# Kernel optimization log

Hardware: AMD Instinct MI355X
Metric: run time of the kernel (lower is better)

The kernel has to match this reference:

```python
import jax, jax.numpy as jnp
import numpy as np

NS, BS, U, NR, NT, D = 256, 7, 8, 4, 8, 2
ITERS, HID = 3, 200
P, NOISE = 100.0, 1e-7
CIN = 2 * NT * D  # block input width: flattened Z1 and Z2


def setup_inputs() -> dict:
    key = jax.random.key(0)
    ks = jax.random.split(key, 21)
    rn = lambda k, s: jax.random.normal(k, s, dtype=jnp.float32)
    inp = {
        'H_re': rn(ks[0], (NS, BS, BS, U, NR, NT)),
        'H_im': rn(ks[1], (NS, BS, BS, U, NR, NT)),
        'V_re': rn(ks[2], (NS, BS, U, NT, D)),
        'V_im': rn(ks[3], (NS, BS, U, NT, D)),
        'w': jnp.ones((U,), jnp.float32),
        'W1_re': rn(ks[4], (ITERS, HID, CIN)) * 0.05,
        'W1_im': rn(ks[5], (ITERS, HID, CIN)) * 0.05,
        'b1_re': rn(ks[6], (ITERS, HID)) * 0.05,
        'b1_im': rn(ks[7], (ITERS, HID)) * 0.05,
        'W2_re': rn(ks[8], (ITERS, HID, HID)) * 0.05,
        'W2_im': rn(ks[9], (ITERS, HID, HID)) * 0.05,
        'b2_re': rn(ks[10], (ITERS, HID)) * 0.05,
        'b2_im': rn(ks[11], (ITERS, HID)) * 0.05,
        'W3_re': rn(ks[12], (ITERS, HID, HID)) * 0.05,
        'W3_im': rn(ks[13], (ITERS, HID, HID)) * 0.05,
        'b3_re': rn(ks[14], (ITERS, HID)) * 0.05,
        'b3_im': rn(ks[15], (ITERS, HID)) * 0.05,
        'W4_re': rn(ks[16], (ITERS, 1, HID)) * 0.05,
        'W4_im': rn(ks[17], (ITERS, 1, HID)) * 0.05,
        'b4_re': rn(ks[18], (ITERS, 1)) * 0.05,
        'b4_im': rn(ks[19], (ITERS, 1)) * 0.05,
    }
    return inp


def _crelu(x):
    # ComplexReLU: relu on real part, imaginary part passes through
    return jax.nn.relu(x.real) + 1j * x.imag


def _clin(x, W, b):
    # torch Linear with complex weights: x @ W.T + b
    return jnp.einsum('...i,oi->...o', x, W) + b


def _iteration(H, V, w, p):
    n = H.shape[0]
    Z = V
    # HV[n,k,l,i,j] = H[n,k,l,i] @ V[n,k,j]  -> [n,BS,BS,U,U,NR,D]
    HV = jnp.einsum('nklirt,nkjtd->nklijrd', H, V)
    ab = jnp.arange(BS)
    au = jnp.arange(U)
    HV2 = HV[:, ab, ab][:, :, au, au]  # HV[:,k,k,i,i] -> [n,BS,U,NR,D]
    # T[n,k,l,i,j] = HV @ HV^H -> [n,BS,BS,U,U,NR,NR]
    T = jnp.einsum('nklijrd,nklijsd->nklijrs', HV, HV.conj())
    I_r = jnp.eye(NR, dtype=HV.dtype)
    # U[n,l,u] = noise*I + sum_{k,j} T[n,k,l,u,j]
    Usum = NOISE * I_r + T.sum(axis=(1, 4))  # [n,BS,U,NR,NR]
    Y = jnp.linalg.solve(Usum, HV2)
    Td = T[:, ab, ab][:, :, au, au]  # T[:,l,l,u,u]
    F = Usum - Td
    Gamma = jnp.einsum('nlurd,nlure->nlude', HV2.conj(), jnp.linalg.solve(F, HV2))
    IG = jnp.eye(D, dtype=HV.dtype) + Gamma  # [n,BS,U,D,D]
    # A[n,l,m,u] = H[n,l,m,u].mH @ Y[n,m,u] -> [n,BS,BS,U,NT,D]
    A = jnp.einsum('nlmurt,nmurd->nlmutd', H.conj(), Y)
    # L[n,l,u] = sum_m A @ IG[m,u] @ A^H -> [n,BS,U,NT,NT]
    L = jnp.einsum('nlmutd,nmude,nlmuse->nluts', A, IG, A.conj())
    All = A[:, ab, ab]  # A[:,l,l] -> [n,BS,U,NT,D]
    Lam = jnp.einsum('nlutd,nlude->nlute', All, IG)
    wv = w.astype(HV.dtype)[None, None, :, None, None]
    Lam = Lam * wv
    L = L * wv
    Z2 = Lam - jnp.einsum('nluts,nlusd->nlutd', L, Z)
    inp = jnp.concatenate([Z.reshape(n, BS, U, NT * D), Z2.reshape(n, BS, U, NT * D)], -1)
    W1, b1, W2, b2, W3, b3, W4, b4 = p
    h = _crelu(_clin(inp, W1, b1))
    h = _crelu(_clin(h, W2, b2))
    h = _crelu(_clin(h, W3, b3))
    step = _clin(h, W4, b4).real  # [n,BS,U,1]
    Vn = Z + step[..., None] * Z2
    fro = (jnp.abs(Vn) ** 2).sum((-2, -1)).sum(2)  # [n,BS]
    scale = jnp.where(fro > P, jnp.sqrt(P / fro), 1.0)
    return Vn * scale[:, :, None, None, None].astype(Vn.dtype)


def reference(H_re, H_im, V_re, V_im, w, W1_re, W1_im, b1_re, b1_im, W2_re, W2_im, b2_re, b2_im, W3_re, W3_im, b3_re, b3_im, W4_re, W4_im, b4_re, b4_im):
    H = (H_re + 1j * H_im).astype(jnp.complex64)
    V = (V_re + 1j * V_im).astype(jnp.complex64)
    # init_input power normalization per (sample, BS)
    fro0 = (jnp.abs(V) ** 2).sum((-2, -1)).sum(2)
    V = V * jnp.sqrt(P / fro0)[:, :, None, None, None].astype(V.dtype)
    c64 = jnp.complex64
    Ws = [(W1_re + 1j * W1_im).astype(c64), (b1_re + 1j * b1_im).astype(c64),
          (W2_re + 1j * W2_im).astype(c64), (b2_re + 1j * b2_im).astype(c64),
          (W3_re + 1j * W3_im).astype(c64), (b3_re + 1j * b3_im).astype(c64),
          (W4_re + 1j * W4_im).astype(c64), (b4_re + 1j * b4_im).astype(c64)]
    for it in range(ITERS):
        p = tuple(a[it] for a in Ws)
        V = _iteration(H, V, w, p)
    return jnp.stack([V.real, V.imag], axis=-1)
```

## Files before the change

### kernel.cpp

```cpp
#include <hip/hip_runtime.h>
#include <math.h>

#define NS 256
#define BS 7
#define UU 8
#define NR 4
#define NT 8
#define DD 2
#define HID 200
#define CIN 32
#define PP 100.0f
#define NOISEF 1e-7f

typedef _Float16 f16x8 __attribute__((ext_vector_type(8)));
typedef float f32x4 __attribute__((ext_vector_type(4)));

#define AST 424
#define AST0 104
#define NTILES 28
#define B1_KC 3
#define B23_KC 13
#define B1_HALVES (B1_KC*NTILES*64*8)
#define B23_HALVES (B23_KC*NTILES*64*8)
#define BITER_HALVES (B1_HALVES + 2*B23_HALVES)

__device__ void chol_solve(const float2 (*A)[NR], const float2 (*B)[DD], float2 (*X)[DD]) {
  float2 L[NR][NR];
  for (int j = 0; j < NR; ++j) {
    float d = A[j][j].x;
    for (int k = 0; k < j; ++k) d -= L[j][k].x * L[j][k].x + L[j][k].y * L[j][k].y;
    float ld = sqrtf(fmaxf(d, 1e-30f));
    L[j][j] = make_float2(ld, 0.f);
    float inv = 1.f / ld;
    for (int i = j + 1; i < NR; ++i) {
      float sr = A[i][j].x, si = A[i][j].y;
      for (int k = 0; k < j; ++k) {
        float2 a = L[i][k], b = L[j][k];
        sr -= a.x * b.x + a.y * b.y;
        si -= a.y * b.x - a.x * b.y;
      }
      L[i][j] = make_float2(sr * inv, si * inv);
    }
  }
  for (int c = 0; c < DD; ++c) {
    float2 z[NR];
    for (int i = 0; i < NR; ++i) {
      float sr = B[i][c].x, si = B[i][c].y;
      for (int k = 0; k < i; ++k) {
        float2 a = L[i][k], zz = z[k];
        sr -= a.x * zz.x - a.y * zz.y;
        si -= a.x * zz.y + a.y * zz.x;
      }
      float inv = 1.f / L[i][i].x;
      z[i] = make_float2(sr * inv, si * inv);
    }
    for (int i = NR - 1; i >= 0; --i) {
      float sr = z[i].x, si = z[i].y;
      for (int k = i + 1; k < NR; ++k) {
        float2 a = L[k][i], xx = X[k][c];
        sr -= a.x * xx.x + a.y * xx.y;
        si -= a.x * xx.y - a.y * xx.x;
      }
      float inv = 1.f / L[i][i].x;
      X[i][c] = make_float2(sr * inv, si * inv);
    }
  }
}

__global__ void k_norm0(const float* __restrict__ Vre, const float* __restrict__ Vim,
                        float2* __restrict__ Vcur) {
  int nl = blockIdx.x;
  int tid = threadIdx.x;
  size_t base = (size_t)nl * 128;
  float re = Vre[base + tid], im = Vim[base + tid];
  float p = re * re + im * im;
  p += __shfl_down(p, 32); p += __shfl_down(p, 16); p += __shfl_down(p, 8);
  p += __shfl_down(p, 4);  p += __shfl_down(p, 2);  p += __shfl_down(p, 1);
  __shared__ float sred[2];
  if ((tid & 63) == 0) sred[tid >> 6] = p;
  __syncthreads();
  float fro = sred[0] + sred[1];
  float sc = sqrtf(PP / fro);
  Vcur[base + tid] = make_float2(re * sc, im * sc);
}

__global__ __launch_bounds__(512) void k_hv(const float* __restrict__ Hre,
    const float* __restrict__ Him, const float2* __restrict__ Vcur,
    float2* __restrict__ Gsb, float2* __restrict__ Tdb, float2* __restrict__ HV2b) {
  int nl = blockIdx.x; int l = nl % BS; int n = nl / BS;
  int tid = threadIdx.x;
  int wave = tid >> 6;
  int lane = tid & 63;
  int k = lane >> 3, j = lane & 7;

  __shared__ float2 Hs[1820];
  __shared__ float2 Vs[952];

  for (int idx = tid; idx < 1792; idx += 512) {
    int kk = idx >> 8, irt = idx & 255;
    size_t off = ((size_t)(n * BS + kk) * BS + l) * 256 + irt;
    Hs[kk * 260 + irt] = make_float2(Hre[off], Him[off]);
  }
  const float2* Vn = Vcur + (size_t)n * 896;
  for (int idx = tid; idx < 896; idx += 512) {
    int kj = idx >> 4, td = idx & 15;
    Vs[kj * 17 + td] = Vn[idx];
  }
  __syncthreads();

  float2 Gu[10];
  #pragma unroll
  for (int q = 0; q < 10; ++q) Gu[q] = make_float2(0.f, 0.f);
  float2 hv[4][2];
  #pragma unroll
  for (int r = 0; r < 4; ++r)
    #pragma unroll
    for (int d = 0; d < 2; ++d) hv[r][d] = make_float2(0.f, 0.f);

  if (k < 7) {
    float2 v[8][2];
    const float2* vp = &Vs[(k * 8 + j) * 17];
    #pragma unroll
    for (int t = 0; t < 8; ++t) { v[t][0] = vp[2 * t]; v[t][1] = vp[2 * t + 1]; }
    #pragma unroll
    for (int r = 0; r < 4; ++r) {
      const float2* hp = &Hs[k * 260 + wave * 32 + r * 8];
      #pragma unroll
      for (int t = 0; t < 8; ++t) {
        float2 h = hp[t];
        #pragma unroll
        for (int d = 0; d < 2; ++d) {
          hv[r][d].x += h.x * v[t][d].x - h.y * v[t][d].y;
          hv[r][d].y += h.x * v[t][d].y + h.y * v[t][d].x;
        }
      }
    }
    int ui = 0;
    #pragma unroll
    for (int r = 0; r < 4; ++r)
      #pragma unroll
      for (int s = r; s < 4; ++s) {
        float gr = 0.f, gi = 0.f;
        #pragma unroll
        for (int d = 0; d < 2; ++d) {
          float2 a = hv[r][d], c = hv[s][d];
          gr += a.x * c.x + a.y * c.y;
          gi += a.y * c.x - a.x * c.y;
        }
        Gu[ui] = make_float2(gr, gi);
        ++ui;
      }
  }
  if (k == l && j == wave) {
    float2* tdp = Tdb + (size_t)(nl * 8 + wave) * 10;
    #pragma unroll
    for (int q = 0; q < 10; ++q) tdp[q] = Gu[q];
    float2* h2p = HV2b + (size_t)(nl * 8 + wave) * 8;
    #pragma unroll
    for (int x = 0; x < 8; ++x) h2p[x] = hv[x >> 1][x & 1];
  }
  #pragma unroll
  for (int m = 1; m < 64; m <<= 1) {
    #pragma unroll
    for (int q = 0; q < 10; ++q) {
      Gu[q].x += __shfl_xor(Gu[q].x, m);
      Gu[q].y += __shfl_xor(Gu[q].y, m);
    }
  }
  if (lane == 0) {
    float2* gp = Gsb + (size_t)(nl * 8 + wave) * 10;
    #pragma unroll
    for (int q = 0; q < 10; ++q) gp[q] = Gu[q];
  }
}

__global__ __launch_bounds__(256) void k_solve(const float2* __restrict__ Gsb,
    const float2* __restrict__ Tdb, const float2* __restrict__ HV2b,
    float2* __restrict__ Yb, float2* __restrict__ IGb) {
  int gid = blockIdx.x * 256 + threadIdx.x;
  int which = (gid >= 14336) ? 1 : 0;
  int b = gid - which * 14336;

  float2 G[10];
  const float2* gp = Gsb + (size_t)b * 10;
  #pragma unroll
  for (int q = 0; q < 10; ++q) G[q] = gp[q];
  if (which) {
    const float2* tp = Tdb + (size_t)b * 10;
    #pragma unroll
    for (int q = 0; q < 10; ++q) { float2 t = tp[q]; G[q].x -= t.x; G[q].y -= t.y; }
  }
  float2 M[NR][NR];
  {
    int ui = 0;
    #pragma unroll
    for (int r = 0; r < 4; ++r)
      #pragma unroll
      for (int s = r; s < 4; ++s) {
        M[r][s] = G[ui];
        M[s][r] = make_float2(G[ui].x, -G[ui].y);
        ++ui;
      }
    #pragma unroll
    for (int r = 0; r < 4; ++r) { M[r][r].x += NOISEF; M[r][r].y = 0.f; }
  }
  float2 Bv[NR][DD], X[NR][DD];
  const float2* hp = HV2b + (size_t)b * 8;
  #pragma unroll
  for (int x = 0; x < 8; ++x) Bv[x >> 1][x & 1] = hp[x];
  chol_solve(M, Bv, X);
  if (!which) {
    #pragma unroll
    for (int x = 0; x < 8; ++x) Yb[(size_t)b * 8 + x] = X[x >> 1][x & 1];
  } else {
    #pragma unroll
    for (int d = 0; d < DD; ++d)
      #pragma unroll
      for (int e = 0; e < DD; ++e) {
        float gr = (d == e) ? 1.f : 0.f, gi = 0.f;
        #pragma unroll
        for (int r = 0; r < NR; ++r) {
          float2 a = Bv[r][d], x = X[r][e];
          gr += a.x * x.x + a.y * x.y;
          gi += a.x * x.y - a.y * x.x;
        }
        IGb[(size_t)b * 4 + d * 2 + e] = make_float2(gr, gi);
      }
  }
}

__global__ __launch_bounds__(256) void k_stage2(const float* __restrict__ Hre,
    const float* __restrict__ Him, const float2* __restrict__ Vcur,
    const float2* __restrict__ Yb, const float2* __restrict__ IGb,
    const float* __restrict__ w, float2* __restrict__ Z2out) {
  int nl = blockIdx.x; int l = nl % BS; int n = nl / BS;
  int tid = threadIdx.x;
  __shared__ float2 SM[3686];
  float2* Hsm  = SM;
  float2* Bsm  = SM;
  float2* Lsm  = SM + 952;
  float2* Ysm  = SM + 1792;
  float2* IGsm = SM + 2247;
  float2* Asm  = SM + 2478;
  float2* Lamm = SM + 3430;
  float2* Zlm  = SM + 3558;

  size_t hbase = ((size_t)n * BS + l) * 1792;
  for (int idx = tid; idx < 1792; idx += 256) {
    int t = idx & 7, r = (idx >> 3) & 3, u = (idx >> 5) & 7, m = idx >> 8;
    Hsm[((u * 4 + r) * 7 + m) * 8 + t] = make_float2(Hre[hbase + idx], Him[hbase + idx]);
  }
  const float2* yp = Yb + (size_t)n * 448;
  for (int idx = tid; idx < 448; idx += 256)
    Ysm[(idx >> 6) * 65 + (idx & 63)] = yp[idx];
  const float2* igp = IGb + (size_t)n * 224;
  if (tid < 224) IGsm[(tid >> 5) * 33 + (tid & 31)] = igp[tid];
  const float2* zp = Vcur + (size_t)nl * 128;
  if (tid < 128) Zlm[tid] = zp[tid];
  __syncthreads();

  for (int idx = tid; idx < 896; idx += 256) {
    int u = idx / 112, rem = idx % 112, m = rem >> 4, t = (rem >> 1) & 7, d = rem & 1;
    float ar = 0.f, ai = 0.f;
    #pragma unroll
    for (int r = 0; r < NR; ++r) {
      float2 h = Hsm[((u * 4 + r) * 7 + m) * 8 + t];
      float2 y = Ysm[m * 65 + u * 8 + r * 2 + d];
      ar += h.x * y.x + h.y * y.y;
      ai += h.x * y.y - h.y * y.x;
    }
    Asm[u * 119 + m * 17 + t * 2 + d] = make_float2(ar, ai);
  }
  __syncthreads();

  for (int idx = tid; idx < 896; idx += 256) {
    int u = idx / 112, rem = idx % 112, m = rem >> 4, t = (rem >> 1) & 7, e = rem & 1;
    float br = 0.f, bi = 0.f;
    #pragma unroll
    for (int d = 0; d < DD; ++d) {
      float2 a = Asm[u * 119 + m * 17 + t * 2 + d];
      float2 g = IGsm[m * 33 + u * 4 + d * 2 + e];
      br += a.x * g.x - a.y * g.y;
      bi += a.x * g.y + a.y * g.x;
    }
    Bsm[u * 119 + m * 17 + t * 2 + e] = make_float2(br, bi);
  }
  __syncthreads();

  for (int idx = tid; idx < 512; idx += 256) {
    int u = idx >> 6, t = (idx >> 3) & 7, s = idx & 7;
    float lr = 0.f, li = 0.f;
    #pragma unroll
    for (int m = 0; m < BS; ++m)
      #pragma unroll
      for (int e = 0; e < DD; ++e) {
        float2 bb = Bsm[u * 119 + m * 17 + t * 2 + e];
        float2 ac = Asm[u * 119 + m * 17 + s * 2 + e];
        lr += bb.x * ac.x + bb.y * ac.y;
        li += bb.y * ac.x - bb.x * ac.y;
      }
    float wu = w[u];
    Lsm[(u * 8 + t) * 8 + s] = make_float2(lr * wu, li * wu);
  }
  if (tid < 128) {
    int u = tid >> 4, t = (tid >> 1) & 7, e = tid & 1;
    float ar = 0.f, ai = 0.f;
    #pragma unroll
    for (int d = 0; d < DD; ++d) {
      float2 a = Asm[u * 119 + l * 17 + t * 2 + d];
      float2 g = IGsm[l * 33 + u * 4 + d * 2 + e];
      ar += a.x * g.x - a.y * g.y;
      ai += a.x * g.y + a.y * g.x;
    }
    float wu = w[u];
    Lamm[u * 16 + t * 2 + e] = make_float2(ar * wu, ai * wu);
  }
  __syncthreads();

  if (tid < 128) {
    int u = tid >> 4, t = (tid >> 1) & 7, d = tid & 1;
    float2 lam = Lamm[u * 16 + t * 2 + d];
    float zr = lam.x, zi = lam.y;
    #pragma unroll
    for (int s = 0; s < NT; ++s) {
      float2 Lts = Lsm[(u * 8 + t) * 8 + s];
      float2 z = Zlm[u * 16 + s * 2 + d];
      zr -= Lts.x * z.x - Lts.y * z.y;
      zi -= Lts.x * z.y + Lts.y * z.x;
    }
    Z2out[(size_t)nl * 128 + u * 16 + t * 2 + d] = make_float2(zr, zi);
  }
}

__global__ __launch_bounds__(256) void k_pack(
    const float* __restrict__ W1re, const float* __restrict__ W1im,
    const float* __restrict__ b1re, const float* __restrict__ b1im,
    const float* __restrict__ W2re, const float* __restrict__ W2im,
    const float* __restrict__ b2re, const float* __restrict__ b2im,
    const float* __restrict__ W3re, const float* __restrict__ W3im,
    const float* __restrict__ b3re, const float* __restrict__ b3im,
    _Float16* __restrict__ Bout) {
  int gid = blockIdx.x * 256 + threadIdx.x;
  int lane = gid & 63;
  int rest = gid >> 6;
  int nt = rest % NTILES;
  int id2 = rest / NTILES;
  if (id2 >= 87) return;
  int iter = id2 / 29, kk = id2 % 29;
  int layer, kc;
  if (kk < 3)       { layer = 0; kc = kk; }
  else if (kk < 16) { layer = 1; kc = kk - 3; }
  else              { layer = 2; kc = kk - 16; }
  const float *Wr, *Wi, *br, *bi;
  if (layer == 0) { Wr = W1re + iter*HID*CIN; Wi = W1im + iter*HID*CIN; br = b1re + iter*HID; bi = b1im + iter*HID; }
  else if (layer == 1) { Wr = W2re + iter*HID*HID; Wi = W2im + iter*HID*HID; br = b2re + iter*HID; bi = b2im + iter*HID; }
  else { Wr = W3re + iter*HID*HID; Wi = W3im + iter*HID*HID; br = b3re + iter*HID; bi = b3im + iter*HID; }
  int c = nt * 16 + (lane & 15);
  int o = c >> 1; int odd = c & 1;
  f16x8 frag;
  #pragma unroll
  for (int j = 0; j < 8; ++j) {
    int k = kc * 32 + (lane >> 4) * 8 + j;
    float v = 0.f;
    if (o < HID) {
      if (layer == 0) {
        if (k < 32)       v = odd ? Wi[o*32 + k] : Wr[o*32 + k];
        else if (k < 64)  { int i = k - 32; v = odd ? Wr[o*32 + i] : -Wi[o*32 + i]; }
        else if (k == 64) v = odd ? bi[o] : br[o];
      } else {
        if (k < 200)       v = odd ? Wi[o*200 + k] : Wr[o*200 + k];
        else if (k == 207) v = odd ? bi[o] : br[o];
        else if (k >= 208 && k < 408) { int i = k - 208; v = odd ? Wr[o*200 + i] : -Wi[o*200 + i]; }
      }
    }
    frag[j] = (_Float16)v;
  }
  size_t off = (size_t)iter * BITER_HALVES
             + (layer == 0 ? 0 : (layer == 1 ? B1_HALVES : (B1_HALVES + B23_HALVES)))
             + ((size_t)(kc * NTILES + nt) * 64 + lane) * 8;
  *(f16x8*)(Bout + off) = frag;
}

template<int ASTRIDE, int KC>
__device__ inline void do_gemm(const _Float16* Ain,
                               const _Float16* __restrict__ Bg,
                               _Float16* Aout, int wr, int wc, int lane) {
  f32x4 acc[2][7];
  #pragma unroll
  for (int rt = 0; rt < 2; ++rt)
    #pragma unroll
    for (int nt = 0; nt < 7; ++nt)
      acc[rt][nt] = (f32x4){0.f, 0.f, 0.f, 0.f};
  const int r0 = (lane & 15) + wr * 32, g = lane >> 4;
  const _Float16* bp0 = Bg + ((size_t)(wc * 7) * 64 + lane) * 8;
  f16x8 b[7];
  #pragma unroll
  for (int nt = 0; nt < 7; ++nt) b[nt] = *(const f16x8*)(bp0 + nt * 512);
  f16x8 a0 = *(const f16x8*)(Ain + r0 * ASTRIDE + 8 * g);
  f16x8 a1 = *(const f16x8*)(Ain + (r0 + 16) * ASTRIDE + 8 * g);
  #pragma unroll
  for (int kc = 0; kc < KC; ++kc) {
    f16x8 a0n, a1n, bn[7];
    if (kc + 1 < KC) {
      const _Float16* bpn = bp0 + (size_t)(kc + 1) * (NTILES * 512);
      #pragma unroll
      for (int nt = 0; nt < 7; ++nt) bn[nt] = *(const f16x8*)(bpn + nt * 512);
      a0n = *(const f16x8*)(Ain + r0 * ASTRIDE + (kc + 1) * 32 + 8 * g);
      a1n = *(const f16x8*)(Ain + (r0 + 16) * ASTRIDE + (kc + 1) * 32 + 8 * g);
    }
    #pragma unroll
    for (int nt = 0; nt < 7; ++nt) {
      acc[0][nt] = __builtin_amdgcn_mfma_f32_16x16x32_f16(a0, b[nt], acc[0][nt], 0, 0, 0);
      acc[1][nt] = __builtin_amdgcn_mfma_f32_16x16x32_f16(a1, b[nt], acc[1][nt], 0, 0, 0);
    }
    if (kc + 1 < KC) {
      a0 = a0n; a1 = a1n;
      #pragma unroll
      for (int nt = 0; nt < 7; ++nt) b[nt] = bn[nt];
    }
  }
  int cbase = wc * 7 * 16 + (lane & 15);
  #pragma unroll
  for (int nt = 0; nt < 7; ++nt) {
    int c = cbase + nt * 16;
    int o = c >> 1;
    bool isre = !(c & 1);
    if (o < HID) {
      _Float16* outp = Aout + (isre ? o : 208 + o);
      #pragma unroll
      for (int rt = 0; rt < 2; ++rt)
        #pragma unroll
        for (int q = 0; q < 4; ++q) {
          float v = acc[rt][nt][q];
          if (isre) v = fmaxf(v, 0.f);
          outp[(size_t)(wr * 32 + rt * 16 + g * 4 + q) * AST] = (_Float16)v;
        }
    }
  }
}

__global__ __launch_bounds__(512, 2) void k_mlp_mfma(
    const float2* __restrict__ Vcur, const float2* __restrict__ Z2,
    const _Float16* __restrict__ Bp,
    const float* __restrict__ W4re, const float* __restrict__ W4im,
    const float* __restrict__ b4re,
    float2* __restrict__ Vout) {
  int b = blockIdx.x;
  int tid = threadIdx.x;
  int wave = tid >> 6, lane = tid & 63;
  int wr = wave >> 2, wc = wave & 3;

  __shared__ _Float16 A0[64 * AST0];
  __shared__ _Float16 Abuf[2][64 * AST];
  __shared__ float2 Zs[64][16];
  __shared__ float2 Z2s[64][16];
  __shared__ float w4s[2][HID];
  __shared__ float stepv[64];
  __shared__ float scs[8];

  for (int idx = tid; idx < 1024; idx += 512) {
    ((float2*)Zs)[idx]  = Vcur[(size_t)b * 1024 + idx];
    ((float2*)Z2s)[idx] = Z2[(size_t)b * 1024 + idx];
  }
  for (int idx = tid; idx < HID; idx += 512) {
    w4s[0][idx] = W4re[idx];
    w4s[1][idx] = W4im[idx];
  }
  __syncthreads();

  for (int idx = tid; idx < 64 * AST0; idx += 512) {
    int m = idx / AST0, c = idx % AST0;
    float v;
    if (c < 64) {
      int f = c & 31;
      float2 z = (f < 16) ? Zs[m][f] : Z2s[m][f - 16];
      v = (c >= 32) ? z.y : z.x;
    } else v = (c == 64) ? 1.f : 0.f;
    A0[m * AST0 + c] = (_Float16)v;
  }
  for (int idx = tid; idx < 2 * 64 * 16; idx += 512) {
    int buf = idx >> 10, rem = idx & 1023, m = rem >> 4, p = rem & 15;
    int c = (p < 8) ? (200 + p) : (400 + p);
    Abuf[buf][m * AST + c] = (p == 7) ? (_Float16)1.f : (_Float16)0.f;
  }
  __syncthreads();

  do_gemm<AST0, B1_KC>(A0, Bp, &Abuf[0][0], wr, wc, lane);
  __syncthreads();
  do_gemm<AST, B23_KC>(&Abuf[0][0], Bp + B1_HALVES, &Abuf[1][0], wr, wc, lane);
  __syncthreads();
  do_gemm<AST, B23_KC>(&Abuf[1][0], Bp + B1_HALVES + B23_HALVES, &Abuf[0][0], wr, wc, lane);
  __syncthreads();

  {
    int m = tid >> 3, q = tid & 7;
    float acc = 0.f;
    for (int o = q; o < HID; o += 8) {
      float hr = (float)Abuf[0][m * AST + o];
      float hi = (float)Abuf[0][m * AST + 208 + o];
      acc += hr * w4s[0][o] - hi * w4s[1][o];
    }
    acc += __shfl_down(acc, 4, 8);
    acc += __shfl_down(acc, 2, 8);
    acc += __shfl_down(acc, 1, 8);
    if (q == 0) stepv[m] = acc + b4re[0];
  }
  __syncthreads();

  for (int idx = tid; idx < 1024; idx += 512) {
    int m = idx >> 4, f = idx & 15;
    float st = stepv[m];
    float2 z = Zs[m][f], z2 = Z2s[m][f];
    Zs[m][f] = make_float2(fmaf(st, z2.x, z.x), fmaf(st, z2.y, z.y));
  }
  __syncthreads();

  {
    const float2* vp = &Zs[wave * 8][0];
    float2 v0 = vp[lane * 2], v1 = vp[lane * 2 + 1];
    float p = v0.x * v0.x + v0.y * v0.y + v1.x * v1.x + v1.y * v1.y;
    p += __shfl_down(p, 32); p += __shfl_down(p, 16); p += __shfl_down(p, 8);
    p += __shfl_down(p, 4);  p += __shfl_down(p, 2);  p += __shfl_down(p, 1);
    if (lane == 0) scs[wave] = (p > PP) ? sqrtf(PP / p) : 1.f;
  }
  __syncthreads();
  for (int idx = tid; idx < 1024; idx += 512) {
    float sc = scs[idx >> 7];
    float2 v = ((float2*)Zs)[idx];
    Vout[(size_t)b * 1024 + idx] = make_float2(v.x * sc, v.y * sc);
  }
}

extern "C" void kernel_launch(void* const* d_in, const int* in_sizes, int n_in,
                              void* d_out, int out_size, void* d_ws, size_t ws_size,
                              hipStream_t stream) {
  const float* Hre  = (const float*)d_in[0];
  const float* Him  = (const float*)d_in[1];
  const float* Vre  = (const float*)d_in[2];
  const float* Vim  = (const float*)d_in[3];
  const float* w    = (const float*)d_in[4];
  const float* W1re = (const float*)d_in[5];
  const float* W1im = (const float*)d_in[6];
  const float* b1re = (const float*)d_in[7];
  const float* b1im = (const float*)d_in[8];
  const float* W2re = (const float*)d_in[9];
  const float* W2im = (const float*)d_in[10];
  const float* b2re = (const float*)d_in[11];
  const float* b2im = (const float*)d_in[12];
  const float* W3re = (const float*)d_in[13];
  const float* W3im = (const float*)d_in[14];
  const float* b3re = (const float*)d_in[15];
  const float* b3im = (const float*)d_in[16];
  const float* W4re = (const float*)d_in[17];
  const float* W4im = (const float*)d_in[18];
  const float* b4re = (const float*)d_in[19];

  const size_t NV = (size_t)NS * BS * UU * NT * DD;
  const size_t NB = (size_t)NS * BS * UU;
  float2* Vcur = (float2*)d_ws;
  float2* Z2b  = Vcur + NV;
  float2* Yb   = Z2b + NV;
  float2* IGb  = Yb + NB * 8;
  float2* Gsb  = IGb + NB * 4;
  float2* Tdb  = Gsb + NB * 10;
  float2* HV2b = Tdb + NB * 10;
  _Float16* Bpack = (_Float16*)(HV2b + NB * 8);

  k_pack<<<609, 256, 0, stream>>>(W1re, W1im, b1re, b1im, W2re, W2im, b2re, b2im,
                                  W3re, W3im, b3re, b3im, Bpack);
  k_norm0<<<NS * BS, 128, 0, stream>>>(Vre, Vim, Vcur);
  for (int it = 0; it < 3; ++it) {
    k_hv<<<NS * BS, 512, 0, stream>>>(Hre, Him, Vcur, Gsb, Tdb, HV2b);
    k_solve<<<112, 256, 0, stream>>>(Gsb, Tdb, HV2b, Yb, IGb);
    k_stage2<<<NS * BS, 256, 0, stream>>>(Hre, Him, Vcur, Yb, IGb, w, Z2b);
    float2* vout = (it == 2) ? (float2*)d_out : Vcur;
    k_mlp_mfma<<<NS * BS / 8, 512, 0, stream>>>(Vcur, Z2b,
        Bpack + (size_t)it * BITER_HALVES,
        W4re + it * HID, W4im + it * HID, b4re + it, vout);
  }
}
```

Before: 252.1 us.

## Precompute V·V^H Gram per block and form interference covariance via H·C·H^H

Replaces the per-(n,l) HV kernel with two kernels. The first computes C[n,k] = sum_j V V^H (8x8) once per sample and base station. The second forms sum_j HV HV^H as H C H^H per (n,k,l), writing per-k partial sums, and the solve kernel then reduces those partials. This removes the redundant per-user HV product and the 64-lane shuffle reduction. In exchange it adds a kernel launch, a larger partials buffer and tiny 64-thread blocks, and it changes the floating-point summation order.

```diff
diff --git a/kernel.cpp b/kernel.cpp
--- a/kernel.cpp
+++ b/kernel.cpp
@@ -84,97 +84,152 @@
   Vcur[base + tid] = make_float2(re * sc, im * sc);
 }
 
-__global__ __launch_bounds__(512) void k_hv(const float* __restrict__ Hre,
+__global__ __launch_bounds__(448) void k_C(const float2* __restrict__ Vcur,
+    float2* __restrict__ Cb) {
+  int n = blockIdx.x;
+  int tid = threadIdx.x;
+  __shared__ float2 Vs[952];
+  const float2* Vn = Vcur + (size_t)n * 896;
+  for (int idx = tid; idx < 896; idx += 448)
+    Vs[(idx >> 4) * 17 + (idx & 15)] = Vn[idx];
+  __syncthreads();
+  int k = tid >> 6, e = tid & 63, c = e >> 3, t = e & 7;
+  float sr = 0.f, si = 0.f;
+  #pragma unroll
+  for (int j = 0; j < 8; ++j) {
+    const float2* vr = &Vs[(k * 8 + j) * 17];
+    #pragma unroll
+    for (int d = 0; d < 2; ++d) {
+      float2 a = vr[t * 2 + d], b = vr[c * 2 + d];
+      sr += a.x * b.x + a.y * b.y;
+      si += a.y * b.x - a.x * b.y;
+    }
+  }
+  Cb[((size_t)(n * 7 + k) * 8 + c) * 8 + t] = make_float2(sr, si);
+}
+
+__global__ __launch_bounds__(64) void k_gpart(const float* __restrict__ Hre,
     const float* __restrict__ Him, const float2* __restrict__ Vcur,
-    float2* __restrict__ Gsb, float2* __restrict__ Tdb, float2* __restrict__ HV2b) {
-  int nl = blockIdx.x; int l = nl % BS; int n = nl / BS;
-  int tid = threadIdx.x;
-  int wave = tid >> 6;
-  int lane = tid & 63;
-  int k = lane >> 3, j = lane & 7;
-
-  __shared__ float2 Hs[1820];
-  __shared__ float2 Vs[952];
-
-  for (int idx = tid; idx < 1792; idx += 512) {
-    int kk = idx >> 8, irt = idx & 255;
-    size_t off = ((size_t)(n * BS + kk) * BS + l) * 256 + irt;
-    Hs[kk * 260 + irt] = make_float2(Hre[off], Him[off]);
-  }
-  const float2* Vn = Vcur + (size_t)n * 896;
-  for (int idx = tid; idx < 896; idx += 512) {
-    int kj = idx >> 4, td = idx & 15;
-    Vs[kj * 17 + td] = Vn[idx];
-  }
-  __syncthreads();
-
-  float2 Gu[10];
-  #pragma unroll
-  for (int q = 0; q < 10; ++q) Gu[q] = make_float2(0.f, 0.f);
-  float2 hv[4][2];
-  #pragma unroll
-  for (int r = 0; r < 4; ++r)
-    #pragma unroll
-    for (int d = 0; d < 2; ++d) hv[r][d] = make_float2(0.f, 0.f);
-
-  if (k < 7) {
+    const float2* __restrict__ Cb, float2* __restrict__ Gpart,
+    float2* __restrict__ Tdb, float2* __restrict__ HV2b) {
+  int blk = blockIdx.x;
+  int k = blk % 7; int l = (blk / 7) % 7; int n = blk / 49;
+  int lane = threadIdx.x;
+  int i = lane >> 3, c = lane & 7;
+  size_t b_nli = (size_t)n * 56 + l * 8 + i;
+
+  size_t hoff = (((size_t)(n * 7 + k) * 7 + l) * 8 + i) * 32;
+  float hx[4][8], hy[4][8];
+  #pragma unroll
+  for (int r = 0; r < 4; ++r) {
+    float4 a0 = *(const float4*)(Hre + hoff + r * 8);
+    float4 a1 = *(const float4*)(Hre + hoff + r * 8 + 4);
+    float4 b0 = *(const float4*)(Him + hoff + r * 8);
+    float4 b1 = *(const float4*)(Him + hoff + r * 8 + 4);
+    hx[r][0] = a0.x; hx[r][1] = a0.y; hx[r][2] = a0.z; hx[r][3] = a0.w;
+    hx[r][4] = a1.x; hx[r][5] = a1.y; hx[r][6] = a1.z; hx[r][7] = a1.w;
+    hy[r][0] = b0.x; hy[r][1] = b0.y; hy[r][2] = b0.z; hy[r][3] = b0.w;
+    hy[r][4] = b1.x; hy[r][5] = b1.y; hy[r][6] = b1.z; hy[r][7] = b1.w;
+  }
+  float2 Hc[4];
+  #pragma unroll
+  for (int s = 0; s < 4; ++s)
+    Hc[s] = make_float2(Hre[hoff + s * 8 + c], Him[hoff + s * 8 + c]);
+
+  const float2* ct = Cb + ((size_t)(n * 7 + k) * 8 + c) * 8;
+  float2 cc[8];
+  #pragma unroll
+  for (int t2 = 0; t2 < 4; ++t2) {
+    float4 vv = *(const float4*)(ct + t2 * 2);
+    cc[t2 * 2]     = make_float2(vv.x, vv.y);
+    cc[t2 * 2 + 1] = make_float2(vv.z, vv.w);
+  }
+
+  float2 T[4];
+  #pragma unroll
+  for (int r = 0; r < 4; ++r) {
+    float tr = 0.f, ti = 0.f;
+    #pragma unroll
+    for (int t = 0; t < 8; ++t) {
+      tr += hx[r][t] * cc[t].x - hy[r][t] * cc[t].y;
+      ti += hx[r][t] * cc[t].y + hy[r][t] * cc[t].x;
+    }
+    T[r] = make_float2(tr, ti);
+  }
+  float2 G[10];
+  {
+    int ui = 0;
+    #pragma unroll
+    for (int r = 0; r < 4; ++r)
+      #pragma unroll
+      for (int s = r; s < 4; ++s) {
+        float2 a = T[r], hb = Hc[s];
+        G[ui].x = a.x * hb.x + a.y * hb.y;
+        G[ui].y = a.y * hb.x - a.x * hb.y;
+        ++ui;
+      }
+  }
+  #pragma unroll
+  for (int m = 1; m < 8; m <<= 1) {
+    #pragma unroll
+    for (int q = 0; q < 10; ++q) {
+      G[q].x += __shfl_xor(G[q].x, m);
+      G[q].y += __shfl_xor(G[q].y, m);
+    }
+  }
+  if (c == 0) {
+    float2* gp = Gpart + (b_nli * 7 + k) * 10;
+    #pragma unroll
+    for (int q = 0; q < 10; ++q) gp[q] = G[q];
+  }
+
+  if (k == l) {
+    const float2* vp = Vcur + b_nli * 16;
     float2 v[8][2];
-    const float2* vp = &Vs[(k * 8 + j) * 17];
-    #pragma unroll
-    for (int t = 0; t < 8; ++t) { v[t][0] = vp[2 * t]; v[t][1] = vp[2 * t + 1]; }
-    #pragma unroll
-    for (int r = 0; r < 4; ++r) {
-      const float2* hp = &Hs[k * 260 + wave * 32 + r * 8];
-      #pragma unroll
-      for (int t = 0; t < 8; ++t) {
-        float2 h = hp[t];
+    #pragma unroll
+    for (int q = 0; q < 8; ++q) {
+      float4 vv = *(const float4*)(vp + 2 * q);
+      v[q][0] = make_float2(vv.x, vv.y);
+      v[q][1] = make_float2(vv.z, vv.w);
+    }
+    float2 hv[4][2];
+    #pragma unroll
+    for (int r = 0; r < 4; ++r)
+      #pragma unroll
+      for (int d = 0; d < 2; ++d) {
+        float ar = 0.f, ai = 0.f;
         #pragma unroll
-        for (int d = 0; d < 2; ++d) {
-          hv[r][d].x += h.x * v[t][d].x - h.y * v[t][d].y;
-          hv[r][d].y += h.x * v[t][d].y + h.y * v[t][d].x;
+        for (int t = 0; t < 8; ++t) {
+          ar += hx[r][t] * v[t][d].x - hy[r][t] * v[t][d].y;
+          ai += hx[r][t] * v[t][d].y + hy[r][t] * v[t][d].x;
         }
-      }
-    }
-    int ui = 0;
-    #pragma unroll
-    for (int r = 0; r < 4; ++r)
-      #pragma unroll
-      for (int s = r; s < 4; ++s) {
-        float gr = 0.f, gi = 0.f;
+        hv[r][d] = make_float2(ar, ai);
+      }
+    if (c == 0) {
+      float2* tdp = Tdb + b_nli * 10;
+      int ui = 0;
+      #pragma unroll
+      for (int r = 0; r < 4; ++r)
         #pragma unroll
-        for (int d = 0; d < 2; ++d) {
-          float2 a = hv[r][d], c = hv[s][d];
-          gr += a.x * c.x + a.y * c.y;
-          gi += a.y * c.x - a.x * c.y;
+        for (int s = r; s < 4; ++s) {
+          float tr = 0.f, ti = 0.f;
+          #pragma unroll
+          for (int d = 0; d < 2; ++d) {
+            float2 a = hv[r][d], cx = hv[s][d];
+            tr += a.x * cx.x + a.y * cx.y;
+            ti += a.y * cx.x - a.x * cx.y;
+          }
+          tdp[ui] = make_float2(tr, ti);
+          ++ui;
         }
-        Gu[ui] = make_float2(gr, gi);
-        ++ui;
-      }
-  }
-  if (k == l && j == wave) {
-    float2* tdp = Tdb + (size_t)(nl * 8 + wave) * 10;
-    #pragma unroll
-    for (int q = 0; q < 10; ++q) tdp[q] = Gu[q];
-    float2* h2p = HV2b + (size_t)(nl * 8 + wave) * 8;
-    #pragma unroll
-    for (int x = 0; x < 8; ++x) h2p[x] = hv[x >> 1][x & 1];
-  }
-  #pragma unroll
-  for (int m = 1; m < 64; m <<= 1) {
-    #pragma unroll
-    for (int q = 0; q < 10; ++q) {
-      Gu[q].x += __shfl_xor(Gu[q].x, m);
-      Gu[q].y += __shfl_xor(Gu[q].y, m);
-    }
-  }
-  if (lane == 0) {
-    float2* gp = Gsb + (size_t)(nl * 8 + wave) * 10;
-    #pragma unroll
-    for (int q = 0; q < 10; ++q) gp[q] = Gu[q];
-  }
-}
-
-__global__ __launch_bounds__(256) void k_solve(const float2* __restrict__ Gsb,
+      float2* h2p = HV2b + b_nli * 8;
+      #pragma unroll
+      for (int x = 0; x < 8; ++x) h2p[x] = hv[x >> 1][x & 1];
+    }
+  }
+}
+
+__global__ __launch_bounds__(256) void k_solveR(const float2* __restrict__ Gpart,
     const float2* __restrict__ Tdb, const float2* __restrict__ HV2b,
     float2* __restrict__ Yb, float2* __restrict__ IGb) {
   int gid = blockIdx.x * 256 + threadIdx.x;
@@ -182,9 +237,16 @@
   int b = gid - which * 14336;
 
   float2 G[10];
-  const float2* gp = Gsb + (size_t)b * 10;
-  #pragma unroll
-  for (int q = 0; q < 10; ++q) G[q] = gp[q];
+  #pragma unroll
+  for (int q = 0; q < 10; ++q) G[q] = make_float2(0.f, 0.f);
+  const float2* gp = Gpart + (size_t)b * 70;
+  #pragma unroll
+  for (int k = 0; k < 7; ++k)
+    #pragma unroll
+    for (int q = 0; q < 10; ++q) {
+      float2 g = gp[k * 10 + q];
+      G[q].x += g.x; G[q].y += g.y;
+    }
   if (which) {
     const float2* tp = Tdb + (size_t)b * 10;
     #pragma unroll
@@ -561,8 +623,9 @@
   float2* Z2b  = Vcur + NV;
   float2* Yb   = Z2b + NV;
   float2* IGb  = Yb + NB * 8;
-  float2* Gsb  = IGb + NB * 4;
-  float2* Tdb  = Gsb + NB * 10;
+  float2* Cb   = IGb + NB * 4;
+  float2* Gpart= Cb + (size_t)NS * 7 * 64;
+  float2* Tdb  = Gpart + NB * 70;
   float2* HV2b = Tdb + NB * 10;
   _Float16* Bpack = (_Float16*)(HV2b + NB * 8);
 
@@ -570,8 +633,9 @@
                                   W3re, W3im, b3re, b3im, Bpack);
   k_norm0<<<NS * BS, 128, 0, stream>>>(Vre, Vim, Vcur);
   for (int it = 0; it < 3; ++it) {
-    k_hv<<<NS * BS, 512, 0, stream>>>(Hre, Him, Vcur, Gsb, Tdb, HV2b);
-    k_solve<<<112, 256, 0, stream>>>(Gsb, Tdb, HV2b, Yb, IGb);
+    k_C<<<NS, 448, 0, stream>>>(Vcur, Cb);
+    k_gpart<<<NS * BS * BS, 64, 0, stream>>>(Hre, Him, Vcur, Cb, Gpart, Tdb, HV2b);
+    k_solveR<<<112, 256, 0, stream>>>(Gpart, Tdb, HV2b, Yb, IGb);
     k_stage2<<<NS * BS, 256, 0, stream>>>(Hre, Him, Vcur, Yb, IGb, w, Z2b);
     float2* vout = (it == 2) ? (float2*)d_out : Vcur;
     k_mlp_mfma<<<NS * BS / 8, 512, 0, stream>>>(Vcur, Z2b,
```

New measurement: 246.4 us. -2.3%, faster.
